# Performance work log

Hardware: AMD Instinct MI355X
Metric: run time of the kernel (lower is better)

## Reference

```python
import math
import jax, jax.numpy as jnp
import numpy as np

IN_D = 16
H_DIM = 256
NB_STEPS = 50
B = 8192


def _cc_weights(nb_steps):
    # Clenshaw-Curtis quadrature weights and nodes, exactly as the torch code.
    k = np.arange(0, nb_steps + 1, dtype=np.float64).reshape(-1, 1)
    lam = np.cos(k @ k.T * math.pi / nb_steps)
    lam[:, 0] = 0.5
    lam[:, -1] = 0.5 * lam[:, -1]
    lam = lam * 2.0 / nb_steps
    W = np.arange(0, nb_steps + 1, dtype=np.float64).reshape(-1, 1)
    W[1::2] = 0.0
    W = 2.0 / (1.0 - W ** 2)
    W[0] = 1.0
    W[1::2] = 0.0
    cc = (lam.T @ W).astype(np.float32)  # [nb_steps+1, 1]
    steps = np.cos(np.arange(0, nb_steps + 1) * math.pi / nb_steps).astype(np.float32)  # [nb_steps+1]
    return jnp.asarray(cc), jnp.asarray(steps)


def setup_inputs() -> dict:
    key = jax.random.key(0)
    ks = jax.random.split(key, 16)
    s = 0.05
    return {
        "x": jax.random.normal(ks[0], (B, 1), jnp.float32),
        "h": jax.random.normal(ks[1], (B, IN_D - 1), jnp.float32),
        "iw1": jax.random.normal(ks[2], (H_DIM, IN_D), jnp.float32) * s,
        "ib1": jax.random.normal(ks[3], (H_DIM,), jnp.float32) * s,
        "iw2": jax.random.normal(ks[4], (H_DIM, H_DIM), jnp.float32) * s,
        "ib2": jax.random.normal(ks[5], (H_DIM,), jnp.float32) * s,
        "iw3": jax.random.normal(ks[6], (1, H_DIM), jnp.float32) * s,
        "ib3": jax.random.normal(ks[7], (1,), jnp.float32) * s,
        "nw1": jax.random.normal(ks[8], (H_DIM, IN_D - 1), jnp.float32) * s,
        "nb1": jax.random.normal(ks[9], (H_DIM,), jnp.float32) * s,
        "nw2": jax.random.normal(ks[10], (H_DIM, H_DIM), jnp.float32) * s,
        "nb2": jax.random.normal(ks[11], (H_DIM,), jnp.float32) * s,
        "nw3": jax.random.normal(ks[12], (2, H_DIM), jnp.float32) * s,
        "nb3": jax.random.normal(ks[13], (2,), jnp.float32) * s,
        "nb_steps": NB_STEPS,
    }


def _integrand(z, iw1, ib1, iw2, ib2, iw3, ib3):
    # IntegrandNN: Linear-ReLU-Linear-ReLU-Linear-ELU, then +1.0
    a = jax.nn.relu(z @ iw1.T + ib1)
    a = jax.nn.relu(a @ iw2.T + ib2)
    return jax.nn.elu(a @ iw3.T + ib3) + 1.0


def reference(x, h, iw1, ib1, iw2, ib2, iw3, ib3, nw1, nb1, nw2, nb2, nw3, nb3, nb_steps):
    cc, steps = _cc_weights(int(nb_steps))  # cc: [N+1,1], steps: [N+1]
    Bn, n_pts = x.shape[0], int(nb_steps) + 1
    # x0 = 0, so quadrature nodes X_k = x * (steps_k + 1) / 2 -> [B, N+1, 1]
    X = x[:, None, :] * ((steps[None, :, None] + 1.0) * 0.5)
    Xf = X.reshape(-1, 1)                                             # [B*(N+1), 1]
    Hf = jnp.broadcast_to(h[:, None, :], (Bn, n_pts, h.shape[1])).reshape(-1, h.shape[1])
    z = jnp.concatenate([Xf, Hf], axis=1)                             # [B*(N+1), in_d]
    f = _integrand(z, iw1, ib1, iw2, ib2, iw3, ib3).reshape(Bn, n_pts, 1)
    integral = jnp.sum(f * cc[None, :, :], axis=1) * x * 0.5          # [B, 1]
    # conditioner net on h: Linear-ReLU-Linear-ReLU-Linear -> [B, 2]
    a = jax.nn.relu(h @ nw1.T + nb1)
    a = jax.nn.relu(a @ nw2.T + nb2)
    out = a @ nw3.T + nb3
    offset = out[:, :1]
    scaling = jnp.exp(out[:, 1:2])
    return scaling * integral + offset
```

## Files before the change

kernel.cpp:

```cpp
#include <hip/hip_runtime.h>
#include <hip/hip_bf16.h>
#include <math.h>

#define BATCH 8192
#define NPTS  51
#define MTOT  (BATCH*NPTS)

typedef __bf16 bf16x8 __attribute__((ext_vector_type(8)));
typedef float  f32x4  __attribute__((ext_vector_type(4)));

#define OFF_IW2P  0
#define OFF_W1XB  131072
#define OFF_CC    131584
#define OFF_STEPS 131840
#define OFF_OFFS  132096
#define OFF_SCAL  164864
#define OFF_G1B   197632
#define OFF_FVALS 4391936

__device__ __forceinline__ unsigned short f2bf(float f) {
    union { float f; unsigned u; } v; v.f = f;
    unsigned r = v.u + 0x7FFFu + ((v.u >> 16) & 1u);
    return (unsigned short)(r >> 16);
}

__device__ __forceinline__ unsigned pk2bf(float lo, float hi) {
    __hip_bfloat162 t = __float22bfloat162_rn(float2{lo, hi});
    union { __hip_bfloat162 b; unsigned u; } v; v.b = t;
    return v.u;
}

__global__ void k1_fused(const float* __restrict__ iw2, const float* __restrict__ nw1,
                         const float* __restrict__ iw1, const float* __restrict__ ib1,
                         const float* __restrict__ nb1, const float* __restrict__ h,
                         const float* __restrict__ nw2, const float* __restrict__ nb2,
                         const float* __restrict__ nw3, const float* __restrict__ nb3,
                         unsigned short* iw2p, unsigned short* w1xb, float* cc, float* steps,
                         unsigned short* __restrict__ g1b, float* __restrict__ offs,
                         float* __restrict__ scal) {
    int blk = blockIdx.x, tid = threadIdx.x;
    if (blk < 256) {
        int t = blk * 256 + tid;
        int n = t >> 8, k = t & 255;
        int half = n >> 7, nl = n & 127, c = k >> 3, j = k & 7;
        iw2p[half * 32768 + c * 1024 + nl * 8 + j] = f2bf(iw2[t]);
    } else if (blk == 256) {
        w1xb[tid] = f2bf(iw1[tid * 16]);
        const float PI_F = 3.14159265358979323846f;
        if (tid <= 50) {
            int j = tid;
            float s = 0.f;
            for (int i = 0; i <= 50; i += 2) {
                float w = (i == 0) ? 1.f : 2.f / (1.f - (float)(i * i));
                float l;
                if (j == 0 || j == 50) l = 0.5f;
                else { int r = (i * j) % 100; l = __cosf((float)r * (PI_F / 50.f)); }
                s += l * w;
            }
            cc[j]    = s * (2.f / 50.f);
            steps[j] = __cosf((float)j * (PI_F / 50.f));
        }
    } else {
        __shared__ float hs[16][15];
        __shared__ unsigned short a1s[16][264];
        __shared__ float Pp[4 * 2 * 16];
        int b0 = (blk - 257) * 16, n = tid;
        if (tid < 240) { int bb = tid / 15, j = tid % 15; hs[bb][j] = h[(b0 + bb) * 15 + j]; }
        __syncthreads();
        float ir[16], nr[15];
        const float4* ip = (const float4*)(iw1 + n * 16);
        ((float4*)ir)[0] = ip[0]; ((float4*)ir)[1] = ip[1];
        ((float4*)ir)[2] = ip[2]; ((float4*)ir)[3] = ip[3];
        #pragma unroll
        for (int j = 0; j < 15; ++j) nr[j] = nw1[n * 15 + j];
        float bi = ib1[n], bn = nb1[n];
        #pragma unroll
        for (int bb = 0; bb < 16; ++bb) {
            float g = bi, a = bn;
            #pragma unroll
            for (int j = 0; j < 15; ++j) { float hv = hs[bb][j]; g += hv * ir[j + 1]; a += hv * nr[j]; }
            g1b[(b0 + bb) * 256 + n] = f2bf(g);
            a1s[bb][n] = f2bf(fmaxf(a, 0.f));
        }
        __syncthreads();

        int lane = tid & 63, w = tid >> 6, l16 = lane & 15, quad = lane >> 4;
        f32x4 acc[4];
        #pragma unroll
        for (int nt = 0; nt < 4; ++nt) acc[nt] = (f32x4){0.f, 0.f, 0.f, 0.f};
        #pragma unroll
        for (int ks = 0; ks < 8; ++ks) {
            bf16x8 af = *(const bf16x8*)&a1s[l16][ks * 32 + quad * 8];
            #pragma unroll
            for (int nt = 0; nt < 4; ++nt) {
                const float* np = nw2 + (w * 64 + nt * 16 + l16) * 256 + ks * 32 + quad * 8;
                float4 f0 = ((const float4*)np)[0];
                float4 f1 = ((const float4*)np)[1];
                union { uint4 u; bf16x8 v; } bf;
                bf.u.x = pk2bf(f0.x, f0.y); bf.u.y = pk2bf(f0.z, f0.w);
                bf.u.z = pk2bf(f1.x, f1.y); bf.u.w = pk2bf(f1.z, f1.w);
                acc[nt] = __builtin_amdgcn_mfma_f32_16x16x32_bf16(af, bf.v, acc[nt], 0, 0, 0);
            }
        }
        float p0[4], p1[4];
        #pragma unroll
        for (int i = 0; i < 4; ++i) { p0[i] = 0.f; p1[i] = 0.f; }
        #pragma unroll
        for (int nt = 0; nt < 4; ++nt) {
            int nn = w * 64 + nt * 16 + l16;
            float bias = nb2[nn], wa = nw3[nn], wb = nw3[256 + nn];
            #pragma unroll
            for (int i = 0; i < 4; ++i) {
                float v = acc[nt][i] + bias;
                v = v > 0.f ? v : 0.f;
                p0[i] += v * wa;
                p1[i] += v * wb;
            }
        }
        #pragma unroll
        for (int mask = 1; mask < 16; mask <<= 1)
            #pragma unroll
            for (int i = 0; i < 4; ++i) {
                p0[i] += __shfl_xor(p0[i], mask, 64);
                p1[i] += __shfl_xor(p1[i], mask, 64);
            }
        if (l16 == 0) {
            #pragma unroll
            for (int i = 0; i < 4; ++i) {
                int r = quad * 4 + i;
                Pp[w * 32 + r]      = p0[i];
                Pp[w * 32 + 16 + r] = p1[i];
            }
        }
        __syncthreads();
        if (tid < 16) {
            float s0 = Pp[tid]      + Pp[32 + tid] + Pp[64 + tid] + Pp[96 + tid]  + nb3[0];
            float s1 = Pp[16 + tid] + Pp[48 + tid] + Pp[80 + tid] + Pp[112 + tid] + nb3[1];
            offs[b0 + tid] = s0;
            scal[b0 + tid] = __expf(s1);
        }
    }
}

__launch_bounds__(256, 2)
__global__ void k2_main(const float* __restrict__ x, const unsigned short* __restrict__ g1b,
                        const unsigned short* __restrict__ w1xb, const unsigned short* __restrict__ iw2p,
                        const float* __restrict__ ib2, const float* __restrict__ iw3,
                        const float* __restrict__ ib3, const float* __restrict__ cc,
                        const float* __restrict__ steps, float* __restrict__ fvals) {
    __shared__ __align__(16) unsigned char smem[68608];
    float* Pp = (float*)smem;

    int tid = threadIdx.x;
    int m0  = blockIdx.x * 128;
    int lane = tid & 63, w = tid >> 6;
    int mw = w & 1, nw = w >> 1;
    int l16 = lane & 15, quad = lane >> 4;

    unsigned blo = (unsigned)(((unsigned long long)(unsigned)m0 * 657931ull) >> 25);

    int hh = tid >> 7, t7 = tid & 127;
    const unsigned char* bsrc = (const unsigned char*)iw2p + hh * 65536 + t7 * 16;
    unsigned char* bds0 = smem + hh * 16384 + t7 * 16;

    #pragma unroll
    for (int it = 0; it < 8; ++it)
        __builtin_amdgcn_global_load_lds(
            (const __attribute__((address_space(1))) unsigned int*)(bsrc + it * 2048),
            (__attribute__((address_space(3))) unsigned int*)(bds0 + it * 2048),
            16, 0, 0);
    if (tid < 128)
        __builtin_amdgcn_global_load_lds(
            (const __attribute__((address_space(1))) unsigned int*)((const unsigned char*)g1b + blo * 512 + tid * 16),
            (__attribute__((address_space(3))) unsigned int*)(smem + 65536 + tid * 16),
            16, 0, 0);
    else if (tid < 160)
        __builtin_amdgcn_global_load_lds(
            (const __attribute__((address_space(1))) unsigned int*)((const unsigned char*)w1xb + (tid - 128) * 16),
            (__attribute__((address_space(3))) unsigned int*)(smem + 67584 + (tid - 128) * 16),
            16, 0, 0);

    float xs_[4]; int rel_[4];
    #pragma unroll
    for (int mt = 0; mt < 4; ++mt) {
        int m = m0 + mw * 64 + mt * 16 + l16;
        unsigned b = (unsigned)(((unsigned long long)(unsigned)m * 657931ull) >> 25);
        int p = m - (int)b * 51;
        xs_[mt] = x[b] * (steps[p] + 1.f) * 0.5f;
        rel_[mt] = (int)(b - blo) * 256;
    }

    f32x4 acc[4][8];
    #pragma unroll
    for (int mt = 0; mt < 4; ++mt)
        #pragma unroll
        for (int nt = 0; nt < 8; ++nt)
            acc[mt][nt] = (f32x4){0.f, 0.f, 0.f, 0.f};

    const unsigned short* AgB = (const unsigned short*)(smem + 65536);
    const unsigned short* WlB = (const unsigned short*)(smem + 67584);

    #pragma unroll
    for (int kc = 0; kc < 4; ++kc) {
        __syncthreads();
        if (kc < 3) {
            const unsigned char* s2 = bsrc + (kc + 1) * 16384;
            unsigned char* d2 = smem + ((kc + 1) & 1) * 32768 + hh * 16384 + t7 * 16;
            #pragma unroll
            for (int it = 0; it < 8; ++it)
                __builtin_amdgcn_global_load_lds(
                    (const __attribute__((address_space(1))) unsigned int*)(s2 + it * 2048),
                    (__attribute__((address_space(3))) unsigned int*)(d2 + it * 2048),
                    16, 0, 0);
        }
        const unsigned short* Bl = (const unsigned short*)(smem + (kc & 1) * 32768) + nw * 8192;
        #pragma unroll
        for (int s = 0; s < 2; ++s) {
            int ks = kc * 2 + s;
            int ko = ks * 32 + quad * 8;
            int cl = s * 4 + quad;

            bf16x8 wv = *(const bf16x8*)(WlB + ko);
            float wl0 = (float)wv[0], wl1 = (float)wv[1], wl2 = (float)wv[2], wl3 = (float)wv[3];
            float wl4 = (float)wv[4], wl5 = (float)wv[5], wl6 = (float)wv[6], wl7 = (float)wv[7];

            union { uint4 u; bf16x8 v; } af[4];
            #pragma unroll
            for (int mt = 0; mt < 4; ++mt) {
                bf16x8 gv = *(const bf16x8*)(AgB + rel_[mt] + ko);
                float xs = xs_[mt];
                float a0 = fmaxf(fmaf(xs, wl0, (float)gv[0]), 0.f);
                float a1 = fmaxf(fmaf(xs, wl1, (float)gv[1]), 0.f);
                float a2 = fmaxf(fmaf(xs, wl2, (float)gv[2]), 0.f);
                float a3 = fmaxf(fmaf(xs, wl3, (float)gv[3]), 0.f);
                float a4 = fmaxf(fmaf(xs, wl4, (float)gv[4]), 0.f);
                float a5 = fmaxf(fmaf(xs, wl5, (float)gv[5]), 0.f);
                float a6 = fmaxf(fmaf(xs, wl6, (float)gv[6]), 0.f);
                float a7 = fmaxf(fmaf(xs, wl7, (float)gv[7]), 0.f);
                af[mt].u.x = pk2bf(a0, a1); af[mt].u.y = pk2bf(a2, a3);
                af[mt].u.z = pk2bf(a4, a5); af[mt].u.w = pk2bf(a6, a7);
            }

            #pragma unroll
            for (int g = 0; g < 2; ++g) {
                bf16x8 bfr[4];
                #pragma unroll
                for (int nt = 0; nt < 4; ++nt)
                    bfr[nt] = *(const bf16x8*)(Bl + cl * 1024 + ((g * 4 + nt) * 16 + l16) * 8);
                #pragma unroll
                for (int mt = 0; mt < 4; ++mt)
                    #pragma unroll
                    for (int nt = 0; nt < 4; ++nt)
                        acc[mt][g * 4 + nt] = __builtin_amdgcn_mfma_f32_16x16x32_bf16(
                            af[mt].v, bfr[nt], acc[mt][g * 4 + nt], 0, 0, 0);
            }
        }
    }

    float pf[4][4];
    #pragma unroll
    for (int mt = 0; mt < 4; ++mt)
        #pragma unroll
        for (int i = 0; i < 4; ++i) pf[mt][i] = 0.f;
    #pragma unroll
    for (int nt = 0; nt < 8; ++nt) {
        int n = nw * 128 + nt * 16 + l16;
        float bias = ib2[n], w3 = iw3[n];
        #pragma unroll
        for (int mt = 0; mt < 4; ++mt)
            #pragma unroll
            for (int i = 0; i < 4; ++i) {
                float v = acc[mt][nt][i] + bias;
                v = v > 0.f ? v : 0.f;
                pf[mt][i] += v * w3;
            }
    }
    __syncthreads();
    #pragma unroll
    for (int mt = 0; mt < 4; ++mt)
        #pragma unroll
        for (int i = 0; i < 4; ++i) {
            int row = mw * 64 + mt * 16 + quad * 4 + i;
            Pp[row * 36 + nw * 16 + l16] = pf[mt][i];
        }
    __syncthreads();
    if (tid < 128) {
        const float4* pp = (const float4*)(Pp + tid * 36);
        float4 v0 = pp[0], v1 = pp[1], v2 = pp[2], v3 = pp[3];
        float4 v4 = pp[4], v5 = pp[5], v6 = pp[6], v7 = pp[7];
        float s = v0.x + v0.y + v0.z + v0.w + v1.x + v1.y + v1.z + v1.w
                + v2.x + v2.y + v2.z + v2.w + v3.x + v3.y + v3.z + v3.w
                + v4.x + v4.y + v4.z + v4.w + v5.x + v5.y + v5.z + v5.w
                + v6.x + v6.y + v6.z + v6.w + v7.x + v7.y + v7.z + v7.w;
        s += ib3[0];
        int m = m0 + tid;
        unsigned b = (unsigned)(((unsigned long long)(unsigned)m * 657931ull) >> 25);
        int p = m - (int)b * 51;
        float f = s > 0.f ? s + 1.f : __expf(s);
        fvals[m] = f * cc[p];
    }
}

__global__ void k4_final(const float* __restrict__ x, const float* __restrict__ fvals,
                         const float* __restrict__ offs, const float* __restrict__ scal,
                         float* __restrict__ out) {
    int tid = threadIdx.x;
    int wv = tid >> 6, lane = tid & 63;
    int b = blockIdx.x * 4 + wv;
    float v = (lane < 51) ? fvals[b * 51 + lane] : 0.f;
    #pragma unroll
    for (int mask = 1; mask < 64; mask <<= 1) v += __shfl_xor(v, mask, 64);
    if (lane == 0)
        out[b] = scal[b] * (0.5f * x[b] * v) + offs[b];
}

extern "C" void kernel_launch(void* const* d_in, const int* in_sizes, int n_in,
                              void* d_out, int out_size, void* d_ws, size_t ws_size,
                              hipStream_t stream) {
    const float* x   = (const float*)d_in[0];
    const float* h   = (const float*)d_in[1];
    const float* iw1 = (const float*)d_in[2];
    const float* ib1 = (const float*)d_in[3];
    const float* iw2 = (const float*)d_in[4];
    const float* ib2 = (const float*)d_in[5];
    const float* iw3 = (const float*)d_in[6];
    const float* ib3 = (const float*)d_in[7];
    const float* nw1 = (const float*)d_in[8];
    const float* nb1 = (const float*)d_in[9];
    const float* nw2 = (const float*)d_in[10];
    const float* nb2 = (const float*)d_in[11];
    const float* nw3 = (const float*)d_in[12];
    const float* nb3 = (const float*)d_in[13];
    float* out = (float*)d_out;

    char* ws = (char*)d_ws;
    unsigned short* iw2p = (unsigned short*)(ws + OFF_IW2P);
    unsigned short* w1xb = (unsigned short*)(ws + OFF_W1XB);
    float* cc    = (float*)(ws + OFF_CC);
    float* steps = (float*)(ws + OFF_STEPS);
    float* offs  = (float*)(ws + OFF_OFFS);
    float* scal  = (float*)(ws + OFF_SCAL);
    unsigned short* g1b = (unsigned short*)(ws + OFF_G1B);
    float* fvals = (float*)(ws + OFF_FVALS);

    k1_fused<<<dim3(769), dim3(256), 0, stream>>>(iw2, nw1, iw1, ib1, nb1, h,
                                                  nw2, nb2, nw3, nb3,
                                                  iw2p, w1xb, cc, steps, g1b, offs, scal);
    k2_main<<<dim3(MTOT / 128), dim3(256), 0, stream>>>(x, g1b, w1xb, iw2p, ib2, iw3,
                                                        ib3, cc, steps, fvals);
    k4_final<<<dim3(BATCH / 4), dim3(256), 0, stream>>>(x, fvals, offs, scal, out);
}
```

Before: 169.9 us.

## Split k2 hidden dimension across two blocks and defer ELU to final kernel

k2_main now splits the 256-wide second-layer output across two blocks per 128-row tile. Each block stages only its half of iw2, so LDS use drops from about 68KB to 32KB and the accumulator tile halves, raising the launch bound to 4 blocks per CU. The g1b and w1x fragments are read directly from global memory instead of being staged in LDS. Partial sums go to two buffers, and k4_final combines them and applies bias, ELU and the quadrature weight. The trade-off is recomputing the first-layer activations twice, reading A operands from global memory, and writing an extra fvals buffer.

```diff
diff --git a/kernel.cpp b/kernel.cpp
--- a/kernel.cpp
+++ b/kernel.cpp
@@ -16,7 +16,8 @@
 #define OFF_OFFS  132096
 #define OFF_SCAL  164864
 #define OFF_G1B   197632
-#define OFF_FVALS 4391936
+#define OFF_FV0   4391936
+#define OFF_FV1   6063104
 
 __device__ __forceinline__ unsigned short f2bf(float f) {
     union { float f; unsigned u; } v; v.f = f;
@@ -142,42 +143,30 @@
     }
 }
 
-__launch_bounds__(256, 2)
+__launch_bounds__(256, 4)
 __global__ void k2_main(const float* __restrict__ x, const unsigned short* __restrict__ g1b,
                         const unsigned short* __restrict__ w1xb, const unsigned short* __restrict__ iw2p,
                         const float* __restrict__ ib2, const float* __restrict__ iw3,
-                        const float* __restrict__ ib3, const float* __restrict__ cc,
-                        const float* __restrict__ steps, float* __restrict__ fvals) {
-    __shared__ __align__(16) unsigned char smem[68608];
+                        const float* __restrict__ steps,
+                        float* __restrict__ fv0, float* __restrict__ fv1) {
+    __shared__ __align__(16) unsigned char smem[32768];
     float* Pp = (float*)smem;
 
     int tid = threadIdx.x;
-    int m0  = blockIdx.x * 128;
+    int bid = blockIdx.x;
+    int hf  = bid & 1;
+    int m0  = (bid >> 1) * 128;
     int lane = tid & 63, w = tid >> 6;
     int mw = w & 1, nw = w >> 1;
     int l16 = lane & 15, quad = lane >> 4;
 
-    unsigned blo = (unsigned)(((unsigned long long)(unsigned)m0 * 657931ull) >> 25);
-
-    int hh = tid >> 7, t7 = tid & 127;
-    const unsigned char* bsrc = (const unsigned char*)iw2p + hh * 65536 + t7 * 16;
-    unsigned char* bds0 = smem + hh * 16384 + t7 * 16;
-
-    #pragma unroll
-    for (int it = 0; it < 8; ++it)
+    const unsigned char* bsrc = (const unsigned char*)iw2p + hf * 65536 + tid * 16;
+
+    #pragma unroll
+    for (int it = 0; it < 4; ++it)
         __builtin_amdgcn_global_load_lds(
-            (const __attribute__((address_space(1))) unsigned int*)(bsrc + it * 2048),
-            (__attribute__((address_space(3))) unsigned int*)(bds0 + it * 2048),
-            16, 0, 0);
-    if (tid < 128)
-        __builtin_amdgcn_global_load_lds(
-            (const __attribute__((address_space(1))) unsigned int*)((const unsigned char*)g1b + blo * 512 + tid * 16),
-            (__attribute__((address_space(3))) unsigned int*)(smem + 65536 + tid * 16),
-            16, 0, 0);
-    else if (tid < 160)
-        __builtin_amdgcn_global_load_lds(
-            (const __attribute__((address_space(1))) unsigned int*)((const unsigned char*)w1xb + (tid - 128) * 16),
-            (__attribute__((address_space(3))) unsigned int*)(smem + 67584 + (tid - 128) * 16),
+            (const __attribute__((address_space(1))) unsigned int*)(bsrc + it * 4096),
+            (__attribute__((address_space(3))) unsigned int*)(smem + tid * 16 + it * 4096),
             16, 0, 0);
 
     float xs_[4]; int rel_[4];
@@ -187,47 +176,43 @@
         unsigned b = (unsigned)(((unsigned long long)(unsigned)m * 657931ull) >> 25);
         int p = m - (int)b * 51;
         xs_[mt] = x[b] * (steps[p] + 1.f) * 0.5f;
-        rel_[mt] = (int)(b - blo) * 256;
-    }
-
-    f32x4 acc[4][8];
+        rel_[mt] = (int)b * 256;
+    }
+
+    f32x4 acc[4][4];
     #pragma unroll
     for (int mt = 0; mt < 4; ++mt)
         #pragma unroll
-        for (int nt = 0; nt < 8; ++nt)
+        for (int nt = 0; nt < 4; ++nt)
             acc[mt][nt] = (f32x4){0.f, 0.f, 0.f, 0.f};
-
-    const unsigned short* AgB = (const unsigned short*)(smem + 65536);
-    const unsigned short* WlB = (const unsigned short*)(smem + 67584);
 
     #pragma unroll
     for (int kc = 0; kc < 4; ++kc) {
         __syncthreads();
         if (kc < 3) {
             const unsigned char* s2 = bsrc + (kc + 1) * 16384;
-            unsigned char* d2 = smem + ((kc + 1) & 1) * 32768 + hh * 16384 + t7 * 16;
-            #pragma unroll
-            for (int it = 0; it < 8; ++it)
+            unsigned char* d2 = smem + ((kc + 1) & 1) * 16384 + tid * 16;
+            #pragma unroll
+            for (int it = 0; it < 4; ++it)
                 __builtin_amdgcn_global_load_lds(
-                    (const __attribute__((address_space(1))) unsigned int*)(s2 + it * 2048),
-                    (__attribute__((address_space(3))) unsigned int*)(d2 + it * 2048),
+                    (const __attribute__((address_space(1))) unsigned int*)(s2 + it * 4096),
+                    (__attribute__((address_space(3))) unsigned int*)(d2 + it * 4096),
                     16, 0, 0);
         }
-        const unsigned short* Bl = (const unsigned short*)(smem + (kc & 1) * 32768) + nw * 8192;
+        const unsigned short* Bl = (const unsigned short*)(smem + (kc & 1) * 16384);
         #pragma unroll
         for (int s = 0; s < 2; ++s) {
-            int ks = kc * 2 + s;
-            int ko = ks * 32 + quad * 8;
+            int ko = kc * 64 + s * 32 + quad * 8;
             int cl = s * 4 + quad;
 
-            bf16x8 wv = *(const bf16x8*)(WlB + ko);
+            bf16x8 wv = *(const bf16x8*)(w1xb + ko);
             float wl0 = (float)wv[0], wl1 = (float)wv[1], wl2 = (float)wv[2], wl3 = (float)wv[3];
             float wl4 = (float)wv[4], wl5 = (float)wv[5], wl6 = (float)wv[6], wl7 = (float)wv[7];
 
             union { uint4 u; bf16x8 v; } af[4];
             #pragma unroll
             for (int mt = 0; mt < 4; ++mt) {
-                bf16x8 gv = *(const bf16x8*)(AgB + rel_[mt] + ko);
+                bf16x8 gv = *(const bf16x8*)(g1b + rel_[mt] + ko);
                 float xs = xs_[mt];
                 float a0 = fmaxf(fmaf(xs, wl0, (float)gv[0]), 0.f);
                 float a1 = fmaxf(fmaf(xs, wl1, (float)gv[1]), 0.f);
@@ -242,17 +227,12 @@
             }
 
             #pragma unroll
-            for (int g = 0; g < 2; ++g) {
-                bf16x8 bfr[4];
-                #pragma unroll
-                for (int nt = 0; nt < 4; ++nt)
-                    bfr[nt] = *(const bf16x8*)(Bl + cl * 1024 + ((g * 4 + nt) * 16 + l16) * 8);
+            for (int nt = 0; nt < 4; ++nt) {
+                bf16x8 bfr = *(const bf16x8*)(Bl + cl * 1024 + (nw * 64 + nt * 16 + l16) * 8);
                 #pragma unroll
                 for (int mt = 0; mt < 4; ++mt)
-                    #pragma unroll
-                    for (int nt = 0; nt < 4; ++nt)
-                        acc[mt][g * 4 + nt] = __builtin_amdgcn_mfma_f32_16x16x32_bf16(
-                            af[mt].v, bfr[nt], acc[mt][g * 4 + nt], 0, 0, 0);
+                    acc[mt][nt] = __builtin_amdgcn_mfma_f32_16x16x32_bf16(
+                        af[mt].v, bfr, acc[mt][nt], 0, 0, 0);
             }
         }
     }
@@ -263,8 +243,8 @@
         #pragma unroll
         for (int i = 0; i < 4; ++i) pf[mt][i] = 0.f;
     #pragma unroll
-    for (int nt = 0; nt < 8; ++nt) {
-        int n = nw * 128 + nt * 16 + l16;
+    for (int nt = 0; nt < 4; ++nt) {
+        int n = hf * 128 + nw * 64 + nt * 16 + l16;
         float bias = ib2[n], w3 = iw3[n];
         #pragma unroll
         for (int mt = 0; mt < 4; ++mt)
@@ -292,22 +272,25 @@
                 + v2.x + v2.y + v2.z + v2.w + v3.x + v3.y + v3.z + v3.w
                 + v4.x + v4.y + v4.z + v4.w + v5.x + v5.y + v5.z + v5.w
                 + v6.x + v6.y + v6.z + v6.w + v7.x + v7.y + v7.z + v7.w;
-        s += ib3[0];
-        int m = m0 + tid;
-        unsigned b = (unsigned)(((unsigned long long)(unsigned)m * 657931ull) >> 25);
-        int p = m - (int)b * 51;
-        float f = s > 0.f ? s + 1.f : __expf(s);
-        fvals[m] = f * cc[p];
-    }
-}
-
-__global__ void k4_final(const float* __restrict__ x, const float* __restrict__ fvals,
+        (hf ? fv1 : fv0)[m0 + tid] = s;
+    }
+}
+
+__global__ void k4_final(const float* __restrict__ x, const float* __restrict__ fv0,
+                         const float* __restrict__ fv1, const float* __restrict__ ib3,
+                         const float* __restrict__ cc,
                          const float* __restrict__ offs, const float* __restrict__ scal,
                          float* __restrict__ out) {
     int tid = threadIdx.x;
     int wv = tid >> 6, lane = tid & 63;
     int b = blockIdx.x * 4 + wv;
-    float v = (lane < 51) ? fvals[b * 51 + lane] : 0.f;
+    float v = 0.f;
+    if (lane < 51) {
+        int m = b * 51 + lane;
+        float s = fv0[m] + fv1[m] + ib3[0];
+        float f = s > 0.f ? s + 1.f : __expf(s);
+        v = f * cc[lane];
+    }
     #pragma unroll
     for (int mask = 1; mask < 64; mask <<= 1) v += __shfl_xor(v, mask, 64);
     if (lane == 0)
@@ -341,12 +324,13 @@
     float* offs  = (float*)(ws + OFF_OFFS);
     float* scal  = (float*)(ws + OFF_SCAL);
     unsigned short* g1b = (unsigned short*)(ws + OFF_G1B);
-    float* fvals = (float*)(ws + OFF_FVALS);
+    float* fv0   = (float*)(ws + OFF_FV0);
+    float* fv1   = (float*)(ws + OFF_FV1);
 
     k1_fused<<<dim3(769), dim3(256), 0, stream>>>(iw2, nw1, iw1, ib1, nb1, h,
                                                   nw2, nb2, nw3, nb3,
                                                   iw2p, w1xb, cc, steps, g1b, offs, scal);
-    k2_main<<<dim3(MTOT / 128), dim3(256), 0, stream>>>(x, g1b, w1xb, iw2p, ib2, iw3,
-                                                        ib3, cc, steps, fvals);
-    k4_final<<<dim3(BATCH / 4), dim3(256), 0, stream>>>(x, fvals, offs, scal, out);
-}
+    k2_main<<<dim3((MTOT / 128) * 2), dim3(256), 0, stream>>>(x, g1b, w1xb, iw2p, ib2, iw3,
+                                                              steps, fv0, fv1);
+    k4_final<<<dim3(BATCH / 4), dim3(256), 0, stream>>>(x, fv0, fv1, ib3, cc, offs, scal, out);
+}
```

After: 211.8 us. 1.25x slower.
